# Optimization experiments

Measured on AMD Instinct MI355X. Metric: run time of the kernel, lower is better.

The kernel has to match this reference:

```python
import jax, jax.numpy as jnp
import numpy as np

N = 100000      # nodes
E = 3200000     # directed edges (avg degree 32)
F_IN = 128      # node feature dim
H = 16          # hidden_features
A = 10          # num_actions


def setup_inputs() -> dict:
    key = jax.random.key(0)
    ks = jax.random.split(key, 8)
    x = jax.random.normal(ks[0], (N, F_IN), dtype=jnp.float32)
    edge_index = jax.random.randint(ks[1], (2, E), 0, N, dtype=jnp.int32)
    W1 = jax.random.normal(ks[2], (F_IN, H), dtype=jnp.float32) * (1.0 / np.sqrt(F_IN))
    b1 = jnp.zeros((H,), dtype=jnp.float32)
    W2 = jax.random.normal(ks[3], (H, H), dtype=jnp.float32) * (1.0 / np.sqrt(H))
    b2 = jnp.zeros((H,), dtype=jnp.float32)
    Wc = jax.random.normal(ks[4], (H, A), dtype=jnp.float32) * (1.0 / np.sqrt(H))
    bc = jnp.zeros((A,), dtype=jnp.float32)
    return {"x": x, "edge_index": edge_index, "W1": W1, "b1": b1,
            "W2": W2, "b2": b2, "Wc": Wc, "bc": bc}


def _gcn_norm(edge_index, n_nodes):
    # PyG GCNConv: add self-loops, symmetric normalization deg^-1/2 A_hat deg^-1/2
    loop = jnp.arange(n_nodes, dtype=edge_index.dtype)
    src = jnp.concatenate([edge_index[0], loop])   # message sources
    dst = jnp.concatenate([edge_index[1], loop])   # aggregation targets
    deg = jax.ops.segment_sum(jnp.ones_like(dst, dtype=jnp.float32), dst,
                              num_segments=n_nodes)
    dis = jnp.where(deg > 0, jax.lax.rsqrt(deg), 0.0)  # deg^-1/2, inf -> 0
    norm = dis[src] * dis[dst]                          # [E + N]
    return src, dst, norm


def _gcn_conv(h, W, b, src, dst, norm, n_nodes):
    # transform first (small output dim), then gather/scale/scatter-add
    msg = (h @ W)[src] * norm[:, None]                  # [E+N, out]
    return jax.ops.segment_sum(msg, dst, num_segments=n_nodes) + b


def reference(x, edge_index, W1, b1, W2, b2, Wc, bc):
    n_nodes = x.shape[0]
    src, dst, norm = _gcn_norm(edge_index, n_nodes)
    h = jax.nn.relu(_gcn_conv(x, W1, b1, src, dst, norm, n_nodes))
    # F.dropout(training=False) is identity at inference
    h = jax.nn.relu(_gcn_conv(h, W2, b2, src, dst, norm, n_nodes))
    pooled = jnp.max(h, axis=0)                         # global MaxAggregation -> [H]
    return pooled @ Wc + bc                             # squeeze() -> [A]
```

## Files before the change

kernel.cpp:

```cpp
#include <hip/hip_runtime.h>
#include <hip/hip_fp16.h>


#define FIN 128
#define HDIM 16
#define AOUT 10
#define NPB 256
#define KMAX 512
#define TILE 4096
#define CAP 10240

typedef _Float16 f16x8 __attribute__((ext_vector_type(8)));
typedef float f32x4 __attribute__((ext_vector_type(4)));

__global__ void k_init(int* __restrict__ bcur, unsigned int* __restrict__ pooled,
                       unsigned int* __restrict__ gz, int K) {
    int i = blockIdx.x * 256 + threadIdx.x;
    if (i < K) bcur[i] = i * CAP;
    if (i < 16) pooled[i] = 0u;
    if (i < 8) gz[i] = 0u;
}

__global__ __launch_bounds__(256) void k_bin(const int* __restrict__ src,
                                             const int* __restrict__ dst, int E,
                                             int* __restrict__ bcur,
                                             unsigned int* __restrict__ pairs, int K) {
    __shared__ int hist[KMAX], lofs[KMAX], run[KMAX], gbase[KMAX], ss[256];
    __shared__ unsigned int buf[TILE];
    __shared__ unsigned short bkt[TILE];
    int t = threadIdx.x;
    int e0 = blockIdx.x * TILE;
    int e1 = min(E, e0 + TILE);
    for (int i = t; i < KMAX; i += 256) hist[i] = 0;
    __syncthreads();
    for (int e = e0 + t * 4; e < e1; e += 1024) {
        if (e + 4 <= e1) {
            int4 d4 = *reinterpret_cast<const int4*>(dst + e);
            atomicAdd(&hist[d4.x >> 8], 1);
            atomicAdd(&hist[d4.y >> 8], 1);
            atomicAdd(&hist[d4.z >> 8], 1);
            atomicAdd(&hist[d4.w >> 8], 1);
        } else {
            for (int q = e; q < e1; q++) atomicAdd(&hist[dst[q] >> 8], 1);
        }
    }
    __syncthreads();
    int a0 = hist[2 * t], a1 = hist[2 * t + 1];
    int psum = a0 + a1;
    ss[t] = psum;
    for (int d = 1; d < 256; d <<= 1) {
        __syncthreads();
        int add = (t >= d) ? ss[t - d] : 0;
        __syncthreads();
        ss[t] += add;
    }
    __syncthreads();
    int excl = ss[t] - psum;
    lofs[2 * t] = excl;          run[2 * t] = excl;
    lofs[2 * t + 1] = excl + a0; run[2 * t + 1] = excl + a0;
    __syncthreads();
    for (int b = t; b < K; b += 256)
        if (hist[b]) gbase[b] = atomicAdd(&bcur[b], hist[b]);
    __syncthreads();
    for (int e = e0 + t * 4; e < e1; e += 1024) {
        if (e + 4 <= e1) {
            int4 d4 = *reinterpret_cast<const int4*>(dst + e);
            int4 s4 = *reinterpret_cast<const int4*>(src + e);
            int b, r;
            b = d4.x >> 8; r = atomicAdd(&run[b], 1);
            buf[r] = (unsigned)s4.x | ((unsigned)(d4.x & 255) << 17); bkt[r] = (unsigned short)b;
            b = d4.y >> 8; r = atomicAdd(&run[b], 1);
            buf[r] = (unsigned)s4.y | ((unsigned)(d4.y & 255) << 17); bkt[r] = (unsigned short)b;
            b = d4.z >> 8; r = atomicAdd(&run[b], 1);
            buf[r] = (unsigned)s4.z | ((unsigned)(d4.z & 255) << 17); bkt[r] = (unsigned short)b;
            b = d4.w >> 8; r = atomicAdd(&run[b], 1);
            buf[r] = (unsigned)s4.w | ((unsigned)(d4.w & 255) << 17); bkt[r] = (unsigned short)b;
        } else {
            for (int q = e; q < e1; q++) {
                int d = dst[q], s = src[q], b = d >> 8;
                int r = atomicAdd(&run[b], 1);
                buf[r] = (unsigned)s | ((unsigned)(d & 255) << 17);
                bkt[r] = (unsigned short)b;
            }
        }
    }
    __syncthreads();
    int m = e1 - e0;
    for (int i = t; i < m; i += 256) {
        int b = bkt[i];
        pairs[gbase[b] + i - lofs[b]] = buf[i];
    }
}

__global__ __launch_bounds__(512) void k_sort(const unsigned int* __restrict__ pairs,
                                              const int* __restrict__ bcur,
                                              int* __restrict__ srcidx,
                                              int2* __restrict__ off2,
                                              float* __restrict__ dis, int n) {
    __shared__ int lcnt[NPB], pre[NPB], cur[NPB];
    int b = blockIdx.x, t = threadIdx.x;
    if (t < NPB) lcnt[t] = 0;
    __syncthreads();
    int base = b * CAP;
    int m = bcur[b] - base;
    for (int j = t; j < m; j += 512) atomicAdd(&lcnt[pairs[base + j] >> 17], 1);
    __syncthreads();
    int v = (t < NPB) ? lcnt[t] : 0;
    int w = (v + 3) & ~3;
    if (t < NPB) pre[t] = w;
    for (int d = 1; d < NPB; d <<= 1) {
        __syncthreads();
        int add = (t < NPB && t >= d) ? pre[t - d] : 0;
        __syncthreads();
        if (t < NPB) pre[t] += add;
    }
    __syncthreads();
    if (t < NPB) {
        int start = pre[t] - w;
        cur[t] = start;
        int node = (b << 8) + t;
        if (node < n) {
            off2[node] = make_int2(base + start, base + start + v);
            dis[node] = rsqrtf((float)(v + 1));
        }
        for (int p = v; p < w; p++) srcidx[base + start + p] = n;
    }
    __syncthreads();
    for (int j = t; j < m; j += 512) {
        unsigned p = pairs[base + j];
        int pos = base + atomicAdd(&cur[p >> 17], 1);
        srcidx[pos] = (int)(p & 0x1FFFF);
    }
}

__global__ __launch_bounds__(256) void k_gemm1(const float* __restrict__ x,
                                               const float* __restrict__ W1,
                                               const float* __restrict__ dis,
                                               __half* __restrict__ g16, int n) {
    int l = threadIdx.x & 63;
    int cc = l & 15, kg = l >> 4;
    f16x8 bfrag[4];
#pragma unroll
    for (int kc = 0; kc < 4; kc++)
#pragma unroll
        for (int j = 0; j < 8; j++)
            bfrag[kc][j] = (_Float16)W1[(kc * 32 + kg * 8 + j) * HDIM + cc];
    int tile = blockIdx.x * 4 + (threadIdx.x >> 6);
    int node0 = tile * 16;
    if (node0 >= n) return;
    const float* xr = x + (size_t)(node0 + cc) * FIN;
    f32x4 acc = {0.f, 0.f, 0.f, 0.f};
#pragma unroll
    for (int kc = 0; kc < 4; kc++) {
        float4 xa = *reinterpret_cast<const float4*>(xr + kc * 32 + kg * 8);
        float4 xb = *reinterpret_cast<const float4*>(xr + kc * 32 + kg * 8 + 4);
        f16x8 a;
        a[0] = (_Float16)xa.x; a[1] = (_Float16)xa.y;
        a[2] = (_Float16)xa.z; a[3] = (_Float16)xa.w;
        a[4] = (_Float16)xb.x; a[5] = (_Float16)xb.y;
        a[6] = (_Float16)xb.z; a[7] = (_Float16)xb.w;
        acc = __builtin_amdgcn_mfma_f32_16x16x32_f16(a, bfrag[kc], acc, 0, 0, 0);
    }
#pragma unroll
    for (int i = 0; i < 4; i++) {
        int nd = node0 + kg * 4 + i;
        g16[(size_t)nd * HDIM + cc] = (__half)(dis[nd] * acc[i]);
    }
}

__global__ __launch_bounds__(256) void k_gemm2(const float* __restrict__ h,
                                               const float* __restrict__ W2,
                                               const float* __restrict__ dis,
                                               __half* __restrict__ g16, int n) {
    int l = threadIdx.x & 63;
    int cc = l & 15, kg = l >> 4;
    f16x8 bfrag = {0, 0, 0, 0, 0, 0, 0, 0};
    if (kg < 2) {
#pragma unroll
        for (int j = 0; j < 8; j++)
            bfrag[j] = (_Float16)W2[(kg * 8 + j) * HDIM + cc];
    }
    int tile = blockIdx.x * 4 + (threadIdx.x >> 6);
    int node0 = tile * 16;
    if (node0 >= n) return;
    f16x8 a = {0, 0, 0, 0, 0, 0, 0, 0};
    if (kg < 2) {
        const float* hr = h + (size_t)(node0 + cc) * HDIM + kg * 8;
        float4 xa = *reinterpret_cast<const float4*>(hr);
        float4 xb = *reinterpret_cast<const float4*>(hr + 4);
        a[0] = (_Float16)xa.x; a[1] = (_Float16)xa.y;
        a[2] = (_Float16)xa.z; a[3] = (_Float16)xa.w;
        a[4] = (_Float16)xb.x; a[5] = (_Float16)xb.y;
        a[6] = (_Float16)xb.z; a[7] = (_Float16)xb.w;
    }
    f32x4 acc = {0.f, 0.f, 0.f, 0.f};
    acc = __builtin_amdgcn_mfma_f32_16x16x32_f16(a, bfrag, acc, 0, 0, 0);
#pragma unroll
    for (int i = 0; i < 4; i++) {
        int nd = node0 + kg * 4 + i;
        g16[(size_t)nd * HDIM + cc] = (__half)(dis[nd] * acc[i]);
    }
}

#define ACC4(V) \
    a0 = __hadd2(a0, __builtin_bit_cast(__half2, (V).x)); \
    a1 = __hadd2(a1, __builtin_bit_cast(__half2, (V).y)); \
    a2 = __hadd2(a2, __builtin_bit_cast(__half2, (V).z)); \
    a3 = __hadd2(a3, __builtin_bit_cast(__half2, (V).w));

template <int POOL>
__global__ __launch_bounds__(256) void k_agg16(const __half* __restrict__ g16,
                                               const int2* __restrict__ off2,
                                               const int* __restrict__ srcidx,
                                               const float* __restrict__ dis,
                                               const float* __restrict__ bias,
                                               float* __restrict__ h,
                                               unsigned int* __restrict__ pooled,
                                               int n) {
    __shared__ float smax[4][16];
    int t = threadIdx.x;
    int tid = blockIdx.x * 256 + t;
    int node = tid >> 2, sub = t & 3;
    int piece = sub & 1, half = sub >> 1;
    bool active = node < n;
    float4 o0 = {0.f, 0.f, 0.f, 0.f}, o1 = {0.f, 0.f, 0.f, 0.f};
    if (active) {
        const uint4* gp = reinterpret_cast<const uint4*>(g16);
        int2 oe = off2[node];
        int e0 = oe.x, e1 = oe.y;
        __half2 a0{0, 0}, a1{0, 0}, a2{0, 0}, a3{0, 0};
        if (half == 0) {
            uint4 v = gp[(size_t)node * 2 + piece];
            ACC4(v)
        }
        int e = e0 + 4 * half;
        for (; e + 8 < e1; e += 16) {
            int4 sa = *reinterpret_cast<const int4*>(srcidx + e);
            int4 sb = *reinterpret_cast<const int4*>(srcidx + e + 8);
            uint4 w0 = gp[(size_t)sa.x * 2 + piece];
            uint4 w1 = gp[(size_t)sa.y * 2 + piece];
            uint4 w2 = gp[(size_t)sa.z * 2 + piece];
            uint4 w3 = gp[(size_t)sa.w * 2 + piece];
            uint4 w4 = gp[(size_t)sb.x * 2 + piece];
            uint4 w5 = gp[(size_t)sb.y * 2 + piece];
            uint4 w6 = gp[(size_t)sb.z * 2 + piece];
            uint4 w7 = gp[(size_t)sb.w * 2 + piece];
            ACC4(w0) ACC4(w1) ACC4(w2) ACC4(w3)
            ACC4(w4) ACC4(w5) ACC4(w6) ACC4(w7)
        }
        for (; e < e1; e += 8) {
            int4 sa = *reinterpret_cast<const int4*>(srcidx + e);
            uint4 w0 = gp[(size_t)sa.x * 2 + piece];
            uint4 w1 = gp[(size_t)sa.y * 2 + piece];
            uint4 w2 = gp[(size_t)sa.z * 2 + piece];
            uint4 w3 = gp[(size_t)sa.w * 2 + piece];
            ACC4(w0) ACC4(w1) ACC4(w2) ACC4(w3)
        }
        a0 = __hadd2(a0, __builtin_bit_cast(__half2, __shfl_xor(__builtin_bit_cast(unsigned, a0), 2)));
        a1 = __hadd2(a1, __builtin_bit_cast(__half2, __shfl_xor(__builtin_bit_cast(unsigned, a1), 2)));
        a2 = __hadd2(a2, __builtin_bit_cast(__half2, __shfl_xor(__builtin_bit_cast(unsigned, a2), 2)));
        a3 = __hadd2(a3, __builtin_bit_cast(__half2, __shfl_xor(__builtin_bit_cast(unsigned, a3), 2)));
        if (half == 0) {
            float dn = dis[node];
            const float* bp = bias + piece * 8;
            float2 f0 = __half22float2(a0), f1 = __half22float2(a1);
            float2 f2 = __half22float2(a2), f3 = __half22float2(a3);
            o0.x = fmaxf(dn * f0.x + bp[0], 0.f); o0.y = fmaxf(dn * f0.y + bp[1], 0.f);
            o0.z = fmaxf(dn * f1.x + bp[2], 0.f); o0.w = fmaxf(dn * f1.y + bp[3], 0.f);
            o1.x = fmaxf(dn * f2.x + bp[4], 0.f); o1.y = fmaxf(dn * f2.y + bp[5], 0.f);
            o1.z = fmaxf(dn * f3.x + bp[6], 0.f); o1.w = fmaxf(dn * f3.y + bp[7], 0.f);
            if (!POOL) {
                float4* hp = reinterpret_cast<float4*>(h + (size_t)node * HDIM + piece * 8);
                hp[0] = o0; hp[1] = o1;
            }
        }
    }
    if (POOL) {
#pragma unroll
        for (int d = 4; d <= 32; d <<= 1) {
            o0.x = fmaxf(o0.x, __shfl_xor(o0.x, d)); o0.y = fmaxf(o0.y, __shfl_xor(o0.y, d));
            o0.z = fmaxf(o0.z, __shfl_xor(o0.z, d)); o0.w = fmaxf(o0.w, __shfl_xor(o0.w, d));
            o1.x = fmaxf(o1.x, __shfl_xor(o1.x, d)); o1.y = fmaxf(o1.y, __shfl_xor(o1.y, d));
            o1.z = fmaxf(o1.z, __shfl_xor(o1.z, d)); o1.w = fmaxf(o1.w, __shfl_xor(o1.w, d));
        }
        int wv = t >> 6;
        if ((t & 63) < 2) {
            float* sp = &smax[wv][piece * 8];
            sp[0] = o0.x; sp[1] = o0.y; sp[2] = o0.z; sp[3] = o0.w;
            sp[4] = o1.x; sp[5] = o1.y; sp[6] = o1.z; sp[7] = o1.w;
        }
        __syncthreads();
        if (t < 16) {
            float m = fmaxf(fmaxf(smax[0][t], smax[1][t]), fmaxf(smax[2][t], smax[3][t]));
            atomicMax(&pooled[t], __float_as_uint(m));
        }
    }
}

__global__ void k_final(const unsigned int* __restrict__ pooled, const float* __restrict__ Wc,
                        const float* __restrict__ bc, float* __restrict__ out) {
    __shared__ float p[HDIM];
    int t = threadIdx.x;
    if (t < HDIM) p[t] = __uint_as_float(pooled[t]);
    __syncthreads();
    if (t < AOUT) {
        float acc = bc[t];
#pragma unroll
        for (int c = 0; c < HDIM; c++) acc += p[c] * Wc[c * AOUT + t];
        out[t] = acc;
    }
}

extern "C" void kernel_launch(void* const* d_in, const int* in_sizes, int n_in,
                              void* d_out, int out_size, void* d_ws, size_t ws_size,
                              hipStream_t stream) {
    const float* x  = (const float*)d_in[0];
    const int*   ei = (const int*)d_in[1];
    const float* W1 = (const float*)d_in[2];
    const float* b1 = (const float*)d_in[3];
    const float* W2 = (const float*)d_in[4];
    const float* b2 = (const float*)d_in[5];
    const float* Wc = (const float*)d_in[6];
    const float* bc = (const float*)d_in[7];
    float* out = (float*)d_out;

    int n = in_sizes[0] / FIN;
    int E = in_sizes[1] / 2;
    const int* srcp = ei;
    const int* dstp = ei + E;
    int K = (n + NPB - 1) / NPB;

    char* ws = (char*)d_ws;
    auto alloc = [&](size_t bytes) -> char* {
        char* p = ws;
        ws += (bytes + 255) & ~(size_t)255;
        return p;
    };
    float*        dis   = (float*)alloc((size_t)n * 4);
    int*          bcur  = (int*)alloc((size_t)K * 4);
    int2*         off2  = (int2*)alloc((size_t)n * 8);
    unsigned int* pairs = (unsigned int*)alloc((size_t)K * CAP * 4);
    int*          srcidx= (int*)alloc((size_t)K * CAP * 4);
    __half*       g16   = (__half*)alloc((size_t)(n + 1) * HDIM * 2);
    float*        h     = (float*)alloc((size_t)n * HDIM * 4);
    unsigned int* pooled= (unsigned int*)alloc(64);

    k_init<<<(K + 255) / 256, 256, 0, stream>>>(bcur, pooled,
                                                (unsigned int*)(g16 + (size_t)n * HDIM), K);
    k_bin<<<(E + TILE - 1) / TILE, 256, 0, stream>>>(srcp, dstp, E, bcur, pairs, K);
    k_sort<<<K, 512, 0, stream>>>(pairs, bcur, srcidx, off2, dis, n);

    int ntile = (n + 15) / 16;
    int gblocks = (ntile + 3) / 4;
    k_gemm1<<<gblocks, 256, 0, stream>>>(x, W1, dis, g16, n);
    k_agg16<0><<<(4 * n + 255) / 256, 256, 0, stream>>>(g16, off2, srcidx, dis, b1,
                                                        h, pooled, n);
    k_gemm2<<<gblocks, 256, 0, stream>>>(h, W2, dis, g16, n);
    k_agg16<1><<<(4 * n + 255) / 256, 256, 0, stream>>>(g16, off2, srcidx, dis, b2,
                                                        nullptr, pooled, n);

    k_final<<<1, 64, 0, stream>>>(pooled, Wc, bc, out);
}
```

Before: 137.7 us.

## Fuse second GEMM into first aggregation and cache pairs in registers in sort

The first aggregation kernel now applies bias, ReLU, the 16x16 W2 transform (from LDS, split across lanes and combined with shuffles) and the dis scaling in one pass, writing fp16 g16b directly. This removes the fp32 h round trip and one kernel launch. Separately, k_sort keeps each thread's pairs in a 20-entry register array so the second pass does not reload them from global memory. In exchange it adds register pressure, per-lane FMA work, and a hard assumption that bucket fill never exceeds 20*512 = CAP.

```diff
diff --git a/kernel.cpp b/kernel.cpp
--- a/kernel.cpp
+++ b/kernel.cpp
@@ -14,11 +14,12 @@
 typedef float f32x4 __attribute__((ext_vector_type(4)));
 
 __global__ void k_init(int* __restrict__ bcur, unsigned int* __restrict__ pooled,
-                       unsigned int* __restrict__ gz, int K) {
+                       unsigned int* __restrict__ gza, unsigned int* __restrict__ gzb,
+                       int K) {
     int i = blockIdx.x * 256 + threadIdx.x;
     if (i < K) bcur[i] = i * CAP;
     if (i < 16) pooled[i] = 0u;
-    if (i < 8) gz[i] = 0u;
+    if (i < 8) { gza[i] = 0u; gzb[i] = 0u; }
 }
 
 __global__ __launch_bounds__(256) void k_bin(const int* __restrict__ src,
@@ -103,7 +104,13 @@
     __syncthreads();
     int base = b * CAP;
     int m = bcur[b] - base;
-    for (int j = t; j < m; j += 512) atomicAdd(&lcnt[pairs[base + j] >> 17], 1);
+    unsigned loc[20];
+#pragma unroll
+    for (int q = 0; q < 20; q++) {
+        int j = t + q * 512;
+        loc[q] = (j < m) ? pairs[base + j] : 0u;
+        if (j < m) atomicAdd(&lcnt[loc[q] >> 17], 1);
+    }
     __syncthreads();
     int v = (t < NPB) ? lcnt[t] : 0;
     int w = (v + 3) & ~3;
@@ -126,10 +133,14 @@
         for (int p = v; p < w; p++) srcidx[base + start + p] = n;
     }
     __syncthreads();
-    for (int j = t; j < m; j += 512) {
-        unsigned p = pairs[base + j];
-        int pos = base + atomicAdd(&cur[p >> 17], 1);
-        srcidx[pos] = (int)(p & 0x1FFFF);
+#pragma unroll
+    for (int q = 0; q < 20; q++) {
+        int j = t + q * 512;
+        if (j < m) {
+            unsigned p = loc[q];
+            int pos = base + atomicAdd(&cur[p >> 17], 1);
+            srcidx[pos] = (int)(p & 0x1FFFF);
+        }
     }
 }
 
@@ -168,55 +179,101 @@
     }
 }
 
-__global__ __launch_bounds__(256) void k_gemm2(const float* __restrict__ h,
-                                               const float* __restrict__ W2,
-                                               const float* __restrict__ dis,
-                                               __half* __restrict__ g16, int n) {
-    int l = threadIdx.x & 63;
-    int cc = l & 15, kg = l >> 4;
-    f16x8 bfrag = {0, 0, 0, 0, 0, 0, 0, 0};
-    if (kg < 2) {
-#pragma unroll
-        for (int j = 0; j < 8; j++)
-            bfrag[j] = (_Float16)W2[(kg * 8 + j) * HDIM + cc];
-    }
-    int tile = blockIdx.x * 4 + (threadIdx.x >> 6);
-    int node0 = tile * 16;
-    if (node0 >= n) return;
-    f16x8 a = {0, 0, 0, 0, 0, 0, 0, 0};
-    if (kg < 2) {
-        const float* hr = h + (size_t)(node0 + cc) * HDIM + kg * 8;
-        float4 xa = *reinterpret_cast<const float4*>(hr);
-        float4 xb = *reinterpret_cast<const float4*>(hr + 4);
-        a[0] = (_Float16)xa.x; a[1] = (_Float16)xa.y;
-        a[2] = (_Float16)xa.z; a[3] = (_Float16)xa.w;
-        a[4] = (_Float16)xb.x; a[5] = (_Float16)xb.y;
-        a[6] = (_Float16)xb.z; a[7] = (_Float16)xb.w;
-    }
-    f32x4 acc = {0.f, 0.f, 0.f, 0.f};
-    acc = __builtin_amdgcn_mfma_f32_16x16x32_f16(a, bfrag, acc, 0, 0, 0);
-#pragma unroll
-    for (int i = 0; i < 4; i++) {
-        int nd = node0 + kg * 4 + i;
-        g16[(size_t)nd * HDIM + cc] = (__half)(dis[nd] * acc[i]);
-    }
-}
-
 #define ACC4(V) \
     a0 = __hadd2(a0, __builtin_bit_cast(__half2, (V).x)); \
     a1 = __hadd2(a1, __builtin_bit_cast(__half2, (V).y)); \
     a2 = __hadd2(a2, __builtin_bit_cast(__half2, (V).z)); \
     a3 = __hadd2(a3, __builtin_bit_cast(__half2, (V).w));
 
-template <int POOL>
-__global__ __launch_bounds__(256) void k_agg16(const __half* __restrict__ g16,
-                                               const int2* __restrict__ off2,
-                                               const int* __restrict__ srcidx,
-                                               const float* __restrict__ dis,
-                                               const float* __restrict__ bias,
-                                               float* __restrict__ h,
-                                               unsigned int* __restrict__ pooled,
-                                               int n) {
+#define GATHER_LOOP \
+    int e = e0 + 4 * half; \
+    for (; e + 8 < e1; e += 16) { \
+        int4 sa = *reinterpret_cast<const int4*>(srcidx + e); \
+        int4 sb = *reinterpret_cast<const int4*>(srcidx + e + 8); \
+        uint4 w0 = gp[(size_t)sa.x * 2 + piece]; \
+        uint4 w1 = gp[(size_t)sa.y * 2 + piece]; \
+        uint4 w2 = gp[(size_t)sa.z * 2 + piece]; \
+        uint4 w3 = gp[(size_t)sa.w * 2 + piece]; \
+        uint4 w4 = gp[(size_t)sb.x * 2 + piece]; \
+        uint4 w5 = gp[(size_t)sb.y * 2 + piece]; \
+        uint4 w6 = gp[(size_t)sb.z * 2 + piece]; \
+        uint4 w7 = gp[(size_t)sb.w * 2 + piece]; \
+        ACC4(w0) ACC4(w1) ACC4(w2) ACC4(w3) \
+        ACC4(w4) ACC4(w5) ACC4(w6) ACC4(w7) \
+    } \
+    for (; e < e1; e += 8) { \
+        int4 sa = *reinterpret_cast<const int4*>(srcidx + e); \
+        uint4 w0 = gp[(size_t)sa.x * 2 + piece]; \
+        uint4 w1 = gp[(size_t)sa.y * 2 + piece]; \
+        uint4 w2 = gp[(size_t)sa.z * 2 + piece]; \
+        uint4 w3 = gp[(size_t)sa.w * 2 + piece]; \
+        ACC4(w0) ACC4(w1) ACC4(w2) ACC4(w3) \
+    } \
+    a0 = __hadd2(a0, __builtin_bit_cast(__half2, __shfl_xor(__builtin_bit_cast(unsigned, a0), 2))); \
+    a1 = __hadd2(a1, __builtin_bit_cast(__half2, __shfl_xor(__builtin_bit_cast(unsigned, a1), 2))); \
+    a2 = __hadd2(a2, __builtin_bit_cast(__half2, __shfl_xor(__builtin_bit_cast(unsigned, a2), 2))); \
+    a3 = __hadd2(a3, __builtin_bit_cast(__half2, __shfl_xor(__builtin_bit_cast(unsigned, a3), 2)));
+
+__global__ __launch_bounds__(256) void k_agg_g2(const __half* __restrict__ g16in,
+                                                const int2* __restrict__ off2,
+                                                const int* __restrict__ srcidx,
+                                                const float* __restrict__ dis,
+                                                const float* __restrict__ bias,
+                                                const float* __restrict__ W2,
+                                                __half* __restrict__ g16out, int n) {
+    __shared__ float W2s[HDIM * HDIM];
+    int t = threadIdx.x;
+    W2s[t] = W2[t];
+    __syncthreads();
+    int tid = blockIdx.x * 256 + t;
+    int node = tid >> 2, sub = t & 3;
+    int piece = sub & 1, half = sub >> 1;
+    if (node >= n) return;
+    const uint4* gp = reinterpret_cast<const uint4*>(g16in);
+    int2 oe = off2[node];
+    int e0 = oe.x, e1 = oe.y;
+    __half2 a0{0, 0}, a1{0, 0}, a2{0, 0}, a3{0, 0};
+    if (half == 0) {
+        uint4 v = gp[(size_t)node * 2 + piece];
+        ACC4(v)
+    }
+    GATHER_LOOP
+    float dn = dis[node];
+    const float* bp = bias + piece * 8;
+    float2 f0 = __half22float2(a0), f1 = __half22float2(a1);
+    float2 f2 = __half22float2(a2), f3 = __half22float2(a3);
+    float hreg[8];
+    hreg[0] = fmaxf(dn * f0.x + bp[0], 0.f); hreg[1] = fmaxf(dn * f0.y + bp[1], 0.f);
+    hreg[2] = fmaxf(dn * f1.x + bp[2], 0.f); hreg[3] = fmaxf(dn * f1.y + bp[3], 0.f);
+    hreg[4] = fmaxf(dn * f2.x + bp[4], 0.f); hreg[5] = fmaxf(dn * f2.y + bp[5], 0.f);
+    hreg[6] = fmaxf(dn * f3.x + bp[6], 0.f); hreg[7] = fmaxf(dn * f3.y + bp[7], 0.f);
+    float acc[8];
+    const float* wq = W2s + (piece * 8) * HDIM + half * 8;
+#pragma unroll
+    for (int cc = 0; cc < 8; cc++) {
+        float s = 0.f;
+#pragma unroll
+        for (int jj = 0; jj < 8; jj++) s += hreg[jj] * wq[jj * HDIM + cc];
+        acc[cc] = s;
+    }
+#pragma unroll
+    for (int cc = 0; cc < 8; cc++) acc[cc] += __shfl_xor(acc[cc], 1);
+    if (piece == 0) {
+        __half o[8];
+#pragma unroll
+        for (int cc = 0; cc < 8; cc++) o[cc] = (__half)(dn * acc[cc]);
+        *reinterpret_cast<uint4*>(g16out + (size_t)node * HDIM + half * 8) =
+            *reinterpret_cast<uint4*>(o);
+    }
+}
+
+__global__ __launch_bounds__(256) void k_agg_pool(const __half* __restrict__ g16in,
+                                                  const int2* __restrict__ off2,
+                                                  const int* __restrict__ srcidx,
+                                                  const float* __restrict__ dis,
+                                                  const float* __restrict__ bias,
+                                                  unsigned int* __restrict__ pooled,
+                                                  int n) {
     __shared__ float smax[4][16];
     int t = threadIdx.x;
     int tid = blockIdx.x * 256 + t;
@@ -225,7 +282,7 @@
     bool active = node < n;
     float4 o0 = {0.f, 0.f, 0.f, 0.f}, o1 = {0.f, 0.f, 0.f, 0.f};
     if (active) {
-        const uint4* gp = reinterpret_cast<const uint4*>(g16);
+        const uint4* gp = reinterpret_cast<const uint4*>(g16in);
         int2 oe = off2[node];
         int e0 = oe.x, e1 = oe.y;
         __half2 a0{0, 0}, a1{0, 0}, a2{0, 0}, a3{0, 0};
@@ -233,33 +290,7 @@
             uint4 v = gp[(size_t)node * 2 + piece];
             ACC4(v)
         }
-        int e = e0 + 4 * half;
-        for (; e + 8 < e1; e += 16) {
-            int4 sa = *reinterpret_cast<const int4*>(srcidx + e);
-            int4 sb = *reinterpret_cast<const int4*>(srcidx + e + 8);
-            uint4 w0 = gp[(size_t)sa.x * 2 + piece];
-            uint4 w1 = gp[(size_t)sa.y * 2 + piece];
-            uint4 w2 = gp[(size_t)sa.z * 2 + piece];
-            uint4 w3 = gp[(size_t)sa.w * 2 + piece];
-            uint4 w4 = gp[(size_t)sb.x * 2 + piece];
-            uint4 w5 = gp[(size_t)sb.y * 2 + piece];
-            uint4 w6 = gp[(size_t)sb.z * 2 + piece];
-            uint4 w7 = gp[(size_t)sb.w * 2 + piece];
-            ACC4(w0) ACC4(w1) ACC4(w2) ACC4(w3)
-            ACC4(w4) ACC4(w5) ACC4(w6) ACC4(w7)
-        }
-        for (; e < e1; e += 8) {
-            int4 sa = *reinterpret_cast<const int4*>(srcidx + e);
-            uint4 w0 = gp[(size_t)sa.x * 2 + piece];
-            uint4 w1 = gp[(size_t)sa.y * 2 + piece];
-            uint4 w2 = gp[(size_t)sa.z * 2 + piece];
-            uint4 w3 = gp[(size_t)sa.w * 2 + piece];
-            ACC4(w0) ACC4(w1) ACC4(w2) ACC4(w3)
-        }
-        a0 = __hadd2(a0, __builtin_bit_cast(__half2, __shfl_xor(__builtin_bit_cast(unsigned, a0), 2)));
-        a1 = __hadd2(a1, __builtin_bit_cast(__half2, __shfl_xor(__builtin_bit_cast(unsigned, a1), 2)));
-        a2 = __hadd2(a2, __builtin_bit_cast(__half2, __shfl_xor(__builtin_bit_cast(unsigned, a2), 2)));
-        a3 = __hadd2(a3, __builtin_bit_cast(__half2, __shfl_xor(__builtin_bit_cast(unsigned, a3), 2)));
+        GATHER_LOOP
         if (half == 0) {
             float dn = dis[node];
             const float* bp = bias + piece * 8;
@@ -269,31 +300,25 @@
             o0.z = fmaxf(dn * f1.x + bp[2], 0.f); o0.w = fmaxf(dn * f1.y + bp[3], 0.f);
             o1.x = fmaxf(dn * f2.x + bp[4], 0.f); o1.y = fmaxf(dn * f2.y + bp[5], 0.f);
             o1.z = fmaxf(dn * f3.x + bp[6], 0.f); o1.w = fmaxf(dn * f3.y + bp[7], 0.f);
-            if (!POOL) {
-                float4* hp = reinterpret_cast<float4*>(h + (size_t)node * HDIM + piece * 8);
-                hp[0] = o0; hp[1] = o1;
-            }
-        }
-    }
-    if (POOL) {
-#pragma unroll
-        for (int d = 4; d <= 32; d <<= 1) {
-            o0.x = fmaxf(o0.x, __shfl_xor(o0.x, d)); o0.y = fmaxf(o0.y, __shfl_xor(o0.y, d));
-            o0.z = fmaxf(o0.z, __shfl_xor(o0.z, d)); o0.w = fmaxf(o0.w, __shfl_xor(o0.w, d));
-            o1.x = fmaxf(o1.x, __shfl_xor(o1.x, d)); o1.y = fmaxf(o1.y, __shfl_xor(o1.y, d));
-            o1.z = fmaxf(o1.z, __shfl_xor(o1.z, d)); o1.w = fmaxf(o1.w, __shfl_xor(o1.w, d));
-        }
-        int wv = t >> 6;
-        if ((t & 63) < 2) {
-            float* sp = &smax[wv][piece * 8];
-            sp[0] = o0.x; sp[1] = o0.y; sp[2] = o0.z; sp[3] = o0.w;
-            sp[4] = o1.x; sp[5] = o1.y; sp[6] = o1.z; sp[7] = o1.w;
-        }
-        __syncthreads();
-        if (t < 16) {
-            float m = fmaxf(fmaxf(smax[0][t], smax[1][t]), fmaxf(smax[2][t], smax[3][t]));
-            atomicMax(&pooled[t], __float_as_uint(m));
-        }
+        }
+    }
+#pragma unroll
+    for (int d = 4; d <= 32; d <<= 1) {
+        o0.x = fmaxf(o0.x, __shfl_xor(o0.x, d)); o0.y = fmaxf(o0.y, __shfl_xor(o0.y, d));
+        o0.z = fmaxf(o0.z, __shfl_xor(o0.z, d)); o0.w = fmaxf(o0.w, __shfl_xor(o0.w, d));
+        o1.x = fmaxf(o1.x, __shfl_xor(o1.x, d)); o1.y = fmaxf(o1.y, __shfl_xor(o1.y, d));
+        o1.z = fmaxf(o1.z, __shfl_xor(o1.z, d)); o1.w = fmaxf(o1.w, __shfl_xor(o1.w, d));
+    }
+    int wv = t >> 6;
+    if ((t & 63) < 2) {
+        float* sp = &smax[wv][piece * 8];
+        sp[0] = o0.x; sp[1] = o0.y; sp[2] = o0.z; sp[3] = o0.w;
+        sp[4] = o1.x; sp[5] = o1.y; sp[6] = o1.z; sp[7] = o1.w;
+    }
+    __syncthreads();
+    if (t < 16) {
+        float m = fmaxf(fmaxf(smax[0][t], smax[1][t]), fmaxf(smax[2][t], smax[3][t]));
+        atomicMax(&pooled[t], __float_as_uint(m));
     }
 }
 
@@ -341,23 +366,24 @@
     int2*         off2  = (int2*)alloc((size_t)n * 8);
     unsigned int* pairs = (unsigned int*)alloc((size_t)K * CAP * 4);
     int*          srcidx= (int*)alloc((size_t)K * CAP * 4);
-    __half*       g16   = (__half*)alloc((size_t)(n + 1) * HDIM * 2);
-    float*        h     = (float*)alloc((size_t)n * HDIM * 4);
+    __half*       g16a  = (__half*)alloc((size_t)(n + 1) * HDIM * 2);
+    __half*       g16b  = (__half*)alloc((size_t)(n + 1) * HDIM * 2);
     unsigned int* pooled= (unsigned int*)alloc(64);
 
-    k_init<<<(K + 255) / 256, 256, 0, stream>>>(bcur, pooled,
-                                                (unsigned int*)(g16 + (size_t)n * HDIM), K);
+    k_init<<<(K + 255) / 256, 256, 0, stream>>>(
+        bcur, pooled,
+        (unsigned int*)(g16a + (size_t)n * HDIM),
+        (unsigned int*)(g16b + (size_t)n * HDIM), K);
     k_bin<<<(E + TILE - 1) / TILE, 256, 0, stream>>>(srcp, dstp, E, bcur, pairs, K);
     k_sort<<<K, 512, 0, stream>>>(pairs, bcur, srcidx, off2, dis, n);
 
     int ntile = (n + 15) / 16;
     int gblocks = (ntile + 3) / 4;
-    k_gemm1<<<gblocks, 256, 0, stream>>>(x, W1, dis, g16, n);
-    k_agg16<0><<<(4 * n + 255) / 256, 256, 0, stream>>>(g16, off2, srcidx, dis, b1,
-                                                        h, pooled, n);
-    k_gemm2<<<gblocks, 256, 0, stream>>>(h, W2, dis, g16, n);
-    k_agg16<1><<<(4 * n + 255) / 256, 256, 0, stream>>>(g16, off2, srcidx, dis, b2,
-                                                        nullptr, pooled, n);
+    k_gemm1<<<gblocks, 256, 0, stream>>>(x, W1, dis, g16a, n);
+    k_agg_g2<<<(4 * n + 255) / 256, 256, 0, stream>>>(g16a, off2, srcidx, dis, b1,
+                                                      W2, g16b, n);
+    k_agg_pool<<<(4 * n + 255) / 256, 256, 0, stream>>>(g16b, off2, srcidx, dis, b2,
+                                                        pooled, n);
 
     k_final<<<1, 64, 0, stream>>>(pooled, Wc, bc, out);
 }
```

After: 131.4 us. 4.6% less time.
